# Kernel tuning notes

Measured on AMD Instinct MI355X. Metric: run time of the kernel, lower is better.

## Reference

```python
import jax, jax.numpy as jnp
import numpy as np

N = 65536
E = 1048576
IN_DIM, HID, OUT = 500, 256, 64
ALPHA = 0.1
K = 10


def setup_inputs() -> dict:
    key = jax.random.key(0)
    ks = jax.random.split(key, 12)
    x = jax.random.normal(ks[0], (N, IN_DIM), dtype=jnp.float32)
    edge_row = jax.random.randint(ks[1], (E,), 0, N, dtype=jnp.int32)
    edge_col = jax.random.randint(ks[2], (E,), 0, N, dtype=jnp.int32)
    edge_weight = jax.random.uniform(ks[3], (E,), dtype=jnp.float32)
    # Linear params (Kaiming-uniform-like scale)
    def lin(k, fan_in, fan_out):
        kw, kb = jax.random.split(k)
        bound = 1.0 / np.sqrt(fan_in)
        W = jax.random.uniform(kw, (fan_in, fan_out), minval=-bound, maxval=bound, dtype=jnp.float32)
        b = jax.random.uniform(kb, (fan_out,), minval=-bound, maxval=bound, dtype=jnp.float32)
        return W, b
    W1, b1 = lin(ks[4], IN_DIM, HID)
    W2, b2 = lin(ks[5], HID, HID)
    W3, b3 = lin(ks[6], HID, OUT)
    return {"x": x, "W1": W1, "b1": b1, "W2": W2, "b2": b2,
            "W3": W3, "b3": b3, "edge_weight": edge_weight,
            "edge_row": edge_row, "edge_col": edge_col}


def reference(x, W1, b1, W2, b2, W3, b3, edge_weight, edge_row, edge_col):
    # MLP stack (dropout=0.0, norm_type='none')
    h = jax.nn.relu(x @ W1 + b1)          # [N, HID]
    h = jax.nn.relu(h @ W2 + b2)          # [N, HID]
    h = h @ W3 + b3                        # [N, OUT]
    h0 = h
    w = edge_weight[:, None]               # [E, 1]
    # APPNP: k steps of h = (1-alpha) * (A @ h) + alpha * h0 (SpMM via segment_sum)
    def step(h, _):
        msg = h[edge_col] * w               # [E, OUT] gather + scale
        agg = jax.ops.segment_sum(msg, edge_row, num_segments=N)  # [N, OUT]
        return (1.0 - ALPHA) * agg + ALPHA * h0, None
    h, _ = jax.lax.scan(step, h, None, length=K)
    return h
```

## Files before the change

kernel.cpp:

```cpp
#include <hip/hip_runtime.h>
#include <cstdint>
#include <cstddef>


#define N_NODES   65536
#define N_EDGES   1048576
#define IN_DIM    500
#define IN_PAD    512
#define HID_DIM   256
#define OUT_DIM   64
#define K_STEPS   10

#define NPW   8
#define CAPW  608
#define NCHUNK 16

typedef _Float16 half8 __attribute__((ext_vector_type(8)));
typedef float    f32x4 __attribute__((ext_vector_type(4)));

#define HA_OFF    0ULL
#define HB_OFF    33554432ULL
#define H1_OFF    67108864ULL
#define H0_OFF    67108864ULL
#define H2_OFF    100663296ULL
#define CNT2_OFF  100663296ULL
#define RANK_OFF  104857600ULL
#define TOT_OFF   109051904ULL
#define W1T_OFF   134217728ULL
#define W2T_OFF   134479872ULL
#define W3T_OFF   134610944ULL
#define ROWP_OFF  134643712ULL
#define EDG_OFF   135430400ULL

__device__ __forceinline__ void gload_lds16(const void* g, void* l) {
  __builtin_amdgcn_global_load_lds(
      (const __attribute__((address_space(1))) void*)g,
      (__attribute__((address_space(3))) void*)l, 16, 0, 0);
}

__device__ __forceinline__ float bf2f(unsigned short u) {
  return __uint_as_float(((unsigned)u) << 16);
}
__device__ __forceinline__ unsigned short f2bf_rne(float f) {
  unsigned u = __float_as_uint(f);
  u += 0x7fffu + ((u >> 16) & 1u);
  return (unsigned short)(u >> 16);
}
__device__ __forceinline__ float uaf(int u) {
  return __uint_as_float((unsigned)u);
}
__device__ __forceinline__ float lo16(unsigned v) {
  return __uint_as_float(v << 16);
}
__device__ __forceinline__ float hi16(unsigned v) {
  return __uint_as_float(v & 0xffff0000u);
}

template <int TM, int TN, int WM, int WN, bool RELU, int OMODE>
__global__ __launch_bounds__(256)
void gemm_kernel(const _Float16* __restrict__ A, const _Float16* __restrict__ B,
                 const float* __restrict__ bias, void* __restrict__ Cout,
                 int M, int Nn, int K) {
  static_assert((TM * 8) % 256 == 0 && (TN * 8) % 256 == 0, "tile");
  __shared__ uint4 As[TM * 8];
  __shared__ uint4 Bs[TN * 8];
  const int t    = threadIdx.x;
  const int lane = t & 63;
  const int wave = t >> 6;
  const int wm   = wave / WN;
  const int wn   = wave % WN;
  const int row0 = blockIdx.x * TM;
  const int col0 = blockIdx.y * TN;
  const int l15  = lane & 15;
  const int lq   = lane >> 4;

  f32x4 acc[4][4];
#pragma unroll
  for (int i = 0; i < 4; ++i)
#pragma unroll
    for (int j = 0; j < 4; ++j) acc[i][j] = (f32x4){0.f, 0.f, 0.f, 0.f};

  for (int k0 = 0; k0 < K; k0 += 64) {
#pragma unroll
    for (int i = 0; i < (TM * 8) / 256; ++i) {
      const int c = i * 256 + wave * 64 + lane;
      const int q = c / TM;
      const int r = c % TM;
      gload_lds16(A + (size_t)(row0 + r) * K + (k0 + q * 8),
                  As + i * 256 + wave * 64);
    }
#pragma unroll
    for (int i = 0; i < (TN * 8) / 256; ++i) {
      const int c = i * 256 + wave * 64 + lane;
      const int q = c / TN;
      const int r = c % TN;
      gload_lds16(B + (size_t)(col0 + r) * K + (k0 + q * 8),
                  Bs + i * 256 + wave * 64);
    }
    __syncthreads();
#pragma unroll
    for (int kk = 0; kk < 2; ++kk) {
      const int qa = kk * 4 + lq;
      half8 af[4], bfr[4];
#pragma unroll
      for (int mt = 0; mt < 4; ++mt)
        af[mt] = *((const half8*)(As + (qa * TM + wm * 64 + mt * 16 + l15)));
#pragma unroll
      for (int nt = 0; nt < 4; ++nt)
        bfr[nt] = *((const half8*)(Bs + (qa * TN + wn * 64 + nt * 16 + l15)));
#pragma unroll
      for (int mt = 0; mt < 4; ++mt)
#pragma unroll
        for (int nt = 0; nt < 4; ++nt)
          acc[mt][nt] = __builtin_amdgcn_mfma_f32_16x16x32_f16(
              af[mt], bfr[nt], acc[mt][nt], 0, 0, 0);
    }
    __syncthreads();
  }

#pragma unroll
  for (int mt = 0; mt < 4; ++mt) {
#pragma unroll
    for (int nt = 0; nt < 4; ++nt) {
      const int col = col0 + wn * 64 + nt * 16 + l15;
      const float bv = bias[col];
#pragma unroll
      for (int r = 0; r < 4; ++r) {
        const int row = row0 + wm * 64 + mt * 16 + lq * 4 + r;
        float v = acc[mt][nt][r] + bv;
        if (RELU) v = fmaxf(v, 0.f);
        if (OMODE == 0)
          ((_Float16*)Cout)[(size_t)row * Nn + col] = (_Float16)v;
        else if (OMODE == 1)
          ((unsigned short*)Cout)[(size_t)row * Nn + col] = f2bf_rne(v);
        else
          ((float*)Cout)[(size_t)row * Nn + col] = v;
      }
    }
  }
}

__global__ __launch_bounds__(256)
void gemm1_fused(const float* __restrict__ x, const _Float16* __restrict__ B,
                 const float* __restrict__ bias, _Float16* __restrict__ C) {
  __shared__ uint4 As[64 * 8];
  __shared__ uint4 Bs[256 * 8];
  const int t    = threadIdx.x;
  const int lane = t & 63;
  const int wave = t >> 6;
  const int row0 = blockIdx.x * 64;
  const int l15  = lane & 15;
  const int lq   = lane >> 4;

  f32x4 acc[4][4];
#pragma unroll
  for (int i = 0; i < 4; ++i)
#pragma unroll
    for (int j = 0; j < 4; ++j) acc[i][j] = (f32x4){0.f, 0.f, 0.f, 0.f};

  for (int k0 = 0; k0 < IN_PAD; k0 += 64) {
#pragma unroll
    for (int i = 0; i < 2; ++i) {
      const int c  = i * 256 + t;
      const int q  = c >> 6;
      const int r  = c & 63;
      const int kb = k0 + q * 8;
      const float* src = x + (size_t)(row0 + r) * IN_DIM + kb;
      half8 o;
      if (kb + 8 <= IN_DIM) {
        const float4 a = ((const float4*)src)[0];
        const float4 b = ((const float4*)src)[1];
        o[0] = (_Float16)a.x; o[1] = (_Float16)a.y;
        o[2] = (_Float16)a.z; o[3] = (_Float16)a.w;
        o[4] = (_Float16)b.x; o[5] = (_Float16)b.y;
        o[6] = (_Float16)b.z; o[7] = (_Float16)b.w;
      } else {
#pragma unroll
        for (int jj = 0; jj < 8; ++jj)
          o[jj] = (kb + jj < IN_DIM) ? (_Float16)src[jj] : (_Float16)0.f;
      }
      *(half8*)(As + c) = o;
    }
#pragma unroll
    for (int i = 0; i < 8; ++i) {
      const int c = i * 256 + wave * 64 + lane;
      const int q = c >> 8;
      const int r = c & 255;
      gload_lds16(B + (size_t)r * IN_PAD + (k0 + q * 8),
                  Bs + i * 256 + wave * 64);
    }
    __syncthreads();
#pragma unroll
    for (int kk = 0; kk < 2; ++kk) {
      const int qa = kk * 4 + lq;
      half8 af[4], bfr[4];
#pragma unroll
      for (int mt = 0; mt < 4; ++mt)
        af[mt] = *((const half8*)(As + (qa * 64 + mt * 16 + l15)));
#pragma unroll
      for (int nt = 0; nt < 4; ++nt)
        bfr[nt] = *((const half8*)(Bs + (qa * 256 + wave * 64 + nt * 16 + l15)));
#pragma unroll
      for (int mt = 0; mt < 4; ++mt)
#pragma unroll
        for (int nt = 0; nt < 4; ++nt)
          acc[mt][nt] = __builtin_amdgcn_mfma_f32_16x16x32_f16(
              af[mt], bfr[nt], acc[mt][nt], 0, 0, 0);
    }
    __syncthreads();
  }

#pragma unroll
  for (int mt = 0; mt < 4; ++mt) {
#pragma unroll
    for (int nt = 0; nt < 4; ++nt) {
      const int col = wave * 64 + nt * 16 + l15;
      const float bv = bias[col];
#pragma unroll
      for (int r = 0; r < 4; ++r) {
        const int row = row0 + mt * 16 + lq * 4 + r;
        const float v = fmaxf(acc[mt][nt][r] + bv, 0.f);
        C[(size_t)row * HID_DIM + col] = (_Float16)v;
      }
    }
  }
}

__global__ void cast_w_kernel(const float* __restrict__ W,
                              _Float16* __restrict__ Wt, int K, int Kpad,
                              int Nn) {
  const int idx = blockIdx.x * blockDim.x + threadIdx.x;
  if (idx >= Nn * Kpad) return;
  const int n = idx / Kpad;
  const int k = idx % Kpad;
  const float v = (k < K) ? W[(size_t)k * Nn + n] : 0.f;
  Wt[idx] = (_Float16)v;
}

__global__ void hist2_kernel(const int* __restrict__ row,
                             int* __restrict__ cnt2, int* __restrict__ rank,
                             int E) {
  const int e = blockIdx.x * blockDim.x + threadIdx.x;
  if (e < E)
    rank[e] = atomicAdd(&cnt2[(e >> 16) * N_NODES + row[e]], 1);
}

__global__ void scan_tot_kernel(const int* __restrict__ cnt2,
                                int* __restrict__ tot) {
  const int r = blockIdx.x * blockDim.x + threadIdx.x;
  int s = 0;
#pragma unroll
  for (int c = 0; c < NCHUNK; ++c) s += cnt2[c * N_NODES + r];
  tot[r] = s;
}

__global__ void scan_kernel(const int4* __restrict__ counts4,
                            int* __restrict__ rowptr) {
  __shared__ int part[1024];
  const int t = threadIdx.x;
  const int base = t * 16;
  int4 c[16];
  int s = 0;
#pragma unroll
  for (int i = 0; i < 16; ++i) {
    c[i] = counts4[base + i];
    s += c[i].x + c[i].y + c[i].z + c[i].w;
  }
  part[t] = s;
  __syncthreads();
  for (int off = 1; off < 1024; off <<= 1) {
    const int v = (t >= off) ? part[t - off] : 0;
    __syncthreads();
    part[t] += v;
    __syncthreads();
  }
  int run = (t == 0) ? 0 : part[t - 1];
#pragma unroll
  for (int i = 0; i < 16; ++i) {
    int4 r;
    r.x = run; run += c[i].x;
    r.y = run; run += c[i].y;
    r.z = run; run += c[i].z;
    r.w = run; run += c[i].w;
    ((int4*)rowptr)[base + i] = r;
  }
  if (t == 1023) rowptr[N_NODES] = run;
}

__global__ void chunkbase_kernel(int* __restrict__ cnt2,
                                 const int* __restrict__ rowptr) {
  const int r = blockIdx.x * blockDim.x + threadIdx.x;
  int run = rowptr[r];
#pragma unroll
  for (int c = 0; c < NCHUNK; ++c) {
    const int t = cnt2[c * N_NODES + r];
    cnt2[c * N_NODES + r] = run;
    run += t;
  }
}

__global__ void scatter2_kernel(const int* __restrict__ row,
                                const int* __restrict__ col,
                                const float* __restrict__ w,
                                const int* __restrict__ rank,
                                const int* __restrict__ cbase,
                                int2* __restrict__ edges, int E) {
  const int e = blockIdx.x * blockDim.x + threadIdx.x;
  if (e < E) {
    const int pos = cbase[(e >> 16) * N_NODES + row[e]] + rank[e];
    edges[pos] = make_int2(col[e], __float_as_int(w[e]));
  }
}

template <bool OUT_F32>
__global__ __launch_bounds__(256)
void prop_step(const unsigned short* __restrict__ hin,
               const unsigned short* __restrict__ h0,
               void* __restrict__ hout, const int* __restrict__ rowptr,
               const int2* __restrict__ edges) {
  __shared__ int2 eb[4][CAPW];
  const int wave = threadIdx.x >> 6;
  const int lane = threadIdx.x & 63;
  const int half = lane >> 5;
  const int lp   = lane & 31;
  const int node0 = (blockIdx.x * 4 + wave) * NPW;
  const unsigned* __restrict__ hin32 = (const unsigned*)hin;
  const unsigned* __restrict__ h032  = (const unsigned*)h0;

  const int rp  = rowptr[node0 + min(lane, NPW)];
  const int beg = __shfl(rp, 0);
  const int nE  = __shfl(rp, NPW) - beg;
  const int rrel = rp - beg;
  int2* __restrict__ ebw = eb[wave];

  const bool fast = (nE <= CAPW);
  if (fast) {
    for (int i = lane; i < nE; i += 64) ebw[i] = edges[beg + i];
    __builtin_amdgcn_s_waitcnt(0);
  }

  for (int i = 0; i < NPW; ++i) {
    const int nb = __shfl(rrel, i);
    const int ne = __shfl(rrel, i + 1);
    float ax0 = 0.f, ay0 = 0.f, ax1 = 0.f, ay1 = 0.f;
    int j = nb;
    if (fast) {
      for (; j + 8 <= ne; j += 8) {
        const int2 e0 = ebw[j + 0 + half];
        const int2 e1 = ebw[j + 2 + half];
        const int2 e2 = ebw[j + 4 + half];
        const int2 e3 = ebw[j + 6 + half];
        const unsigned v0 = hin32[(e0.x << 5) | lp];
        const unsigned v1 = hin32[(e1.x << 5) | lp];
        const unsigned v2 = hin32[(e2.x << 5) | lp];
        const unsigned v3 = hin32[(e3.x << 5) | lp];
        const float w0 = uaf(e0.y), w1 = uaf(e1.y);
        const float w2 = uaf(e2.y), w3 = uaf(e3.y);
        ax0 = fmaf(w0, lo16(v0), ax0); ay0 = fmaf(w0, hi16(v0), ay0);
        ax1 = fmaf(w1, lo16(v1), ax1); ay1 = fmaf(w1, hi16(v1), ay1);
        ax0 = fmaf(w2, lo16(v2), ax0); ay0 = fmaf(w2, hi16(v2), ay0);
        ax1 = fmaf(w3, lo16(v3), ax1); ay1 = fmaf(w3, hi16(v3), ay1);
      }
      for (; j + 2 <= ne; j += 2) {
        const int2 e = ebw[j + half];
        const unsigned v = hin32[(e.x << 5) | lp];
        const float w = uaf(e.y);
        ax0 = fmaf(w, lo16(v), ax0); ay0 = fmaf(w, hi16(v), ay0);
      }
      if (j < ne) {
        const int2 e = ebw[j];
        const unsigned v = hin32[(e.x << 5) | lp];
        const float w = half ? 0.f : uaf(e.y);
        ax0 = fmaf(w, lo16(v), ax0); ay0 = fmaf(w, hi16(v), ay0);
      }
    } else {
      for (; j < ne; j += 2) {
        const int idx = j + half;
        const int2 e = edges[beg + (idx < ne ? idx : ne - 1)];
        const float w = (idx < ne) ? uaf(e.y) : 0.f;
        const unsigned v = hin32[(e.x << 5) | lp];
        ax0 = fmaf(w, lo16(v), ax0); ay0 = fmaf(w, hi16(v), ay0);
      }
    }
    float sx = ax0 + ax1;
    float sy = ay0 + ay1;
    sx += __shfl_xor(sx, 32);
    sy += __shfl_xor(sy, 32);
    const int o32 = ((node0 + i) << 5) | lp;
    const unsigned h0v = h032[o32];
    const float r0 = 0.9f * sx + 0.1f * lo16(h0v);
    const float r1 = 0.9f * sy + 0.1f * hi16(h0v);
    if (half == 0) {
      if (OUT_F32) {
        ((float2*)hout)[o32] = make_float2(r0, r1);
      } else {
        ((unsigned*)hout)[o32] =
            (unsigned)f2bf_rne(r0) | ((unsigned)f2bf_rne(r1) << 16);
      }
    }
  }
}

extern "C" void kernel_launch(void* const* d_in, const int* in_sizes, int n_in,
                              void* d_out, int out_size, void* d_ws,
                              size_t ws_size, hipStream_t stream) {
  const float* x  = (const float*)d_in[0];
  const float* W1 = (const float*)d_in[1];
  const float* b1 = (const float*)d_in[2];
  const float* W2 = (const float*)d_in[3];
  const float* b2 = (const float*)d_in[4];
  const float* W3 = (const float*)d_in[5];
  const float* b3 = (const float*)d_in[6];
  const float* ew = (const float*)d_in[7];
  const int* erow = (const int*)d_in[8];
  const int* ecol = (const int*)d_in[9];

  char* ws = (char*)d_ws;
  _Float16* h1  = (_Float16*)(ws + H1_OFF);
  _Float16* h2  = (_Float16*)(ws + H2_OFF);
  _Float16* w1t = (_Float16*)(ws + W1T_OFF);
  _Float16* w2t = (_Float16*)(ws + W2T_OFF);
  _Float16* w3t = (_Float16*)(ws + W3T_OFF);
  unsigned short* h0b = (unsigned short*)(ws + H0_OFF);
  unsigned short* hAb = (unsigned short*)(ws + HA_OFF);
  unsigned short* hBb = (unsigned short*)(ws + HB_OFF);
  int* rowp     = (int*)(ws + ROWP_OFF);
  int* cnt2     = (int*)(ws + CNT2_OFF);
  int* rankb    = (int*)(ws + RANK_OFF);
  int* tot      = (int*)(ws + TOT_OFF);
  int2* edges   = (int2*)(ws + EDG_OFF);
  float* outp   = (float*)d_out;

  hipMemsetAsync(cnt2, 0, NCHUNK * N_NODES * sizeof(int), stream);
  hist2_kernel<<<N_EDGES / 256, 256, 0, stream>>>(erow, cnt2, rankb, N_EDGES);
  scan_tot_kernel<<<N_NODES / 256, 256, 0, stream>>>(cnt2, tot);
  scan_kernel<<<1, 1024, 0, stream>>>((const int4*)tot, rowp);
  chunkbase_kernel<<<N_NODES / 256, 256, 0, stream>>>(cnt2, rowp);
  scatter2_kernel<<<N_EDGES / 256, 256, 0, stream>>>(erow, ecol, ew, rankb,
                                                     cnt2, edges, N_EDGES);

  cast_w_kernel<<<(HID_DIM * IN_PAD) / 256, 256, 0, stream>>>(W1, w1t, IN_DIM,
                                                              IN_PAD, HID_DIM);
  cast_w_kernel<<<(HID_DIM * HID_DIM) / 256, 256, 0, stream>>>(
      W2, w2t, HID_DIM, HID_DIM, HID_DIM);
  cast_w_kernel<<<(OUT_DIM * HID_DIM) / 256, 256, 0, stream>>>(
      W3, w3t, HID_DIM, HID_DIM, OUT_DIM);

  gemm1_fused<<<dim3(N_NODES / 64), 256, 0, stream>>>(x, w1t, b1, h1);
  gemm_kernel<64, 256, 1, 4, true, 0>
      <<<dim3(N_NODES / 64, 1), 256, 0, stream>>>(h1, w2t, b2, h2, N_NODES,
                                                  HID_DIM, HID_DIM);
  gemm_kernel<256, 64, 4, 1, false, 1>
      <<<dim3(N_NODES / 256, 1), 256, 0, stream>>>(h2, w3t, b3, h0b, N_NODES,
                                                   OUT_DIM, HID_DIM);

  for (int s = 0; s < K_STEPS - 1; ++s) {
    const unsigned short* hin = (s == 0) ? h0b : ((s - 1) & 1 ? hBb : hAb);
    unsigned short* hout = (s & 1) ? hBb : hAb;
    prop_step<false><<<N_NODES / (4 * NPW), 256, 0, stream>>>(hin, h0b, hout,
                                                              rowp, edges);
  }
  prop_step<true><<<N_NODES / (4 * NPW), 256, 0, stream>>>(
      (K_STEPS - 2) & 1 ? hBb : hAb, h0b, outp, rowp, edges);
}
```

Measured before the change: 651.4 us.

## Stream fp32 x into LDS asynchronously and convert at fragment load in GEMM1

The first GEMM now copies raw fp32 rows of x straight into shared memory with global_load_lds, instead of loading them through registers and converting to fp16 before the store. The fp16 conversion moves to fragment-read time using packed round-toward-zero converts. The row tile grows to 128, so each block reuses its W1 tile across more rows. The second GEMM switches to a 128x128 tile on a 2D grid. The trade-off is higher register and LDS pressure, plus a small rounding change from RTZ instead of RNE.

```diff
diff --git a/kernel.cpp b/kernel.cpp
--- a/kernel.cpp
+++ b/kernel.cpp
@@ -16,6 +16,7 @@
 #define NCHUNK 16
 
 typedef _Float16 half8 __attribute__((ext_vector_type(8)));
+typedef __fp16   fp16x2 __attribute__((ext_vector_type(2)));
 typedef float    f32x4 __attribute__((ext_vector_type(4)));
 
 #define HA_OFF    0ULL
@@ -38,16 +39,13 @@
       (__attribute__((address_space(3))) void*)l, 16, 0, 0);
 }
 
-__device__ __forceinline__ float bf2f(unsigned short u) {
-  return __uint_as_float(((unsigned)u) << 16);
-}
 __device__ __forceinline__ unsigned short f2bf_rne(float f) {
   unsigned u = __float_as_uint(f);
   u += 0x7fffu + ((u >> 16) & 1u);
   return (unsigned short)(u >> 16);
 }
-__device__ __forceinline__ float uaf(int u) {
-  return __uint_as_float((unsigned)u);
+__device__ __forceinline__ float uaf(unsigned u) {
+  return __uint_as_float(u);
 }
 __device__ __forceinline__ float lo16(unsigned v) {
   return __uint_as_float(v << 16);
@@ -141,77 +139,73 @@
 }
 
 __global__ __launch_bounds__(256)
-void gemm1_fused(const float* __restrict__ x, const _Float16* __restrict__ B,
-                 const float* __restrict__ bias, _Float16* __restrict__ C) {
-  __shared__ uint4 As[64 * 8];
-  __shared__ uint4 Bs[256 * 8];
+void gemm1_f32(const float* __restrict__ x, const _Float16* __restrict__ B,
+               const float* __restrict__ bias, _Float16* __restrict__ C) {
+  __shared__ uint4 As[16 * 128];
+  __shared__ uint4 Bs[8 * 256];
   const int t    = threadIdx.x;
   const int lane = t & 63;
   const int wave = t >> 6;
-  const int row0 = blockIdx.x * 64;
+  const int row0 = blockIdx.x * 128;
   const int l15  = lane & 15;
   const int lq   = lane >> 4;
 
-  f32x4 acc[4][4];
-#pragma unroll
-  for (int i = 0; i < 4; ++i)
+  f32x4 acc[8][4];
+#pragma unroll
+  for (int i = 0; i < 8; ++i)
 #pragma unroll
     for (int j = 0; j < 4; ++j) acc[i][j] = (f32x4){0.f, 0.f, 0.f, 0.f};
 
   for (int k0 = 0; k0 < IN_PAD; k0 += 64) {
 #pragma unroll
-    for (int i = 0; i < 2; ++i) {
-      const int c  = i * 256 + t;
-      const int q  = c >> 6;
-      const int r  = c & 63;
-      const int kb = k0 + q * 8;
-      const float* src = x + (size_t)(row0 + r) * IN_DIM + kb;
-      half8 o;
-      if (kb + 8 <= IN_DIM) {
-        const float4 a = ((const float4*)src)[0];
-        const float4 b = ((const float4*)src)[1];
-        o[0] = (_Float16)a.x; o[1] = (_Float16)a.y;
-        o[2] = (_Float16)a.z; o[3] = (_Float16)a.w;
-        o[4] = (_Float16)b.x; o[5] = (_Float16)b.y;
-        o[6] = (_Float16)b.z; o[7] = (_Float16)b.w;
-      } else {
-#pragma unroll
-        for (int jj = 0; jj < 8; ++jj)
-          o[jj] = (kb + jj < IN_DIM) ? (_Float16)src[jj] : (_Float16)0.f;
-      }
-      *(half8*)(As + c) = o;
-    }
-#pragma unroll
     for (int i = 0; i < 8; ++i) {
-      const int c = i * 256 + wave * 64 + lane;
+      const int c = i * 256 + t;
+      const int q = c >> 7;
+      const int r = c & 127;
+      int kb = k0 + q * 4;
+      if (kb >= IN_DIM) kb = 0;
+      gload_lds16(x + (size_t)(row0 + r) * IN_DIM + kb, As + q * 128 + r);
+    }
+#pragma unroll
+    for (int i = 0; i < 8; ++i) {
+      const int c = i * 256 + t;
       const int q = c >> 8;
       const int r = c & 255;
-      gload_lds16(B + (size_t)r * IN_PAD + (k0 + q * 8),
-                  Bs + i * 256 + wave * 64);
+      gload_lds16(B + (size_t)r * IN_PAD + (k0 + q * 8), Bs + q * 256 + r);
     }
     __syncthreads();
 #pragma unroll
     for (int kk = 0; kk < 2; ++kk) {
       const int qa = kk * 4 + lq;
-      half8 af[4], bfr[4];
-#pragma unroll
-      for (int mt = 0; mt < 4; ++mt)
-        af[mt] = *((const half8*)(As + (qa * 64 + mt * 16 + l15)));
+      half8 bfr[4];
 #pragma unroll
       for (int nt = 0; nt < 4; ++nt)
-        bfr[nt] = *((const half8*)(Bs + (qa * 256 + wave * 64 + nt * 16 + l15)));
-#pragma unroll
-      for (int mt = 0; mt < 4; ++mt)
+        bfr[nt] = *((const half8*)(Bs + qa * 256 + wave * 64 + nt * 16 + l15));
+#pragma unroll
+      for (int mt = 0; mt < 8; ++mt) {
+        const uint4 lo = As[(qa * 2 + 0) * 128 + mt * 16 + l15];
+        const uint4 hi = As[(qa * 2 + 1) * 128 + mt * 16 + l15];
+        half8 af;
+        fp16x2 p;
+        p = __builtin_amdgcn_cvt_pkrtz(uaf(lo.x), uaf(lo.y));
+        af[0] = p[0]; af[1] = p[1];
+        p = __builtin_amdgcn_cvt_pkrtz(uaf(lo.z), uaf(lo.w));
+        af[2] = p[0]; af[3] = p[1];
+        p = __builtin_amdgcn_cvt_pkrtz(uaf(hi.x), uaf(hi.y));
+        af[4] = p[0]; af[5] = p[1];
+        p = __builtin_amdgcn_cvt_pkrtz(uaf(hi.z), uaf(hi.w));
+        af[6] = p[0]; af[7] = p[1];
 #pragma unroll
         for (int nt = 0; nt < 4; ++nt)
           acc[mt][nt] = __builtin_amdgcn_mfma_f32_16x16x32_f16(
-              af[mt], bfr[nt], acc[mt][nt], 0, 0, 0);
-    }
-    __syncthreads();
-  }
-
-#pragma unroll
-  for (int mt = 0; mt < 4; ++mt) {
+              af, bfr[nt], acc[mt][nt], 0, 0, 0);
+      }
+    }
+    __syncthreads();
+  }
+
+#pragma unroll
+  for (int mt = 0; mt < 8; ++mt) {
 #pragma unroll
     for (int nt = 0; nt < 4; ++nt) {
       const int col = wave * 64 + nt * 16 + l15;
@@ -446,10 +440,10 @@
   cast_w_kernel<<<(OUT_DIM * HID_DIM) / 256, 256, 0, stream>>>(
       W3, w3t, HID_DIM, HID_DIM, OUT_DIM);
 
-  gemm1_fused<<<dim3(N_NODES / 64), 256, 0, stream>>>(x, w1t, b1, h1);
-  gemm_kernel<64, 256, 1, 4, true, 0>
-      <<<dim3(N_NODES / 64, 1), 256, 0, stream>>>(h1, w2t, b2, h2, N_NODES,
-                                                  HID_DIM, HID_DIM);
+  gemm1_f32<<<dim3(N_NODES / 128), 256, 0, stream>>>(x, w1t, b1, h1);
+  gemm_kernel<128, 128, 2, 2, true, 0>
+      <<<dim3(N_NODES / 128, HID_DIM / 128), 256, 0, stream>>>(
+          h1, w2t, b2, h2, N_NODES, HID_DIM, HID_DIM);
   gemm_kernel<256, 64, 4, 1, false, 1>
       <<<dim3(N_NODES / 256, 1), 256, 0, stream>>>(h2, w3t, b3, h0b, N_NODES,
                                                    OUT_DIM, HID_DIM);
```

Measured after the change: 629.2 us (median of 2 runs). 3.4% less time.
